# Performance work log

Measured on AMD Instinct MI355X. Metric: run time of the kernel, lower is better.

## Reference

```python
import jax, jax.numpy as jnp
import numpy as np

NS, NP, EJ, ER = 10000, 2048, 32768, 32768  # skills, job/resume pairs, edges
D, H = 1536, 8
NEG_SLOPE_ATT = 0.2   # GAT attention leaky_relu
NEG_SLOPE = 0.01      # F.leaky_relu / nn.LeakyReLU default


def setup_inputs() -> dict:
    key = jax.random.key(0)
    ks = jax.random.split(key, 20)
    rn = lambda k, shp, s=1.0: jax.random.normal(k, shp, dtype=jnp.float32) * s
    s_d = 1.0 / np.sqrt(D)
    return {
        "x_skill": rn(ks[0], (NS, D)),
        "x_job": rn(ks[1], (NP, D)),
        "x_resume": rn(ks[2], (NP, D)),
        # GraphConv params (lin_rel has bias, lin_root bias=False in PyG)
        "W_rel": rn(ks[3], (D, D), s_d),
        "b_rel": jnp.zeros((D,), jnp.float32),
        "W_root": rn(ks[4], (D, D), s_d),
        # GATConv params (heads=8, concat=False)
        "W_gat_src": rn(ks[5], (D, H * D), s_d),
        "W_gat_dst": rn(ks[6], (D, H * D), s_d),
        "att_src": rn(ks[7], (H, D), s_d),
        "att_dst": rn(ks[8], (H, D), s_d),
        "b_gat": jnp.zeros((D,), jnp.float32),
        # MLP: [3072 -> 512 -> 128 -> 1]
        "W1": rn(ks[9], (2 * D, 512), 1.0 / np.sqrt(2 * D)),
        "b1": jnp.zeros((512,), jnp.float32),
        "W2": rn(ks[10], (512, 128), 1.0 / np.sqrt(512)),
        "b2": jnp.zeros((128,), jnp.float32),
        "W3": rn(ks[11], (128, 1), 1.0 / np.sqrt(128)),
        "b3": jnp.zeros((1,), jnp.float32),
        # edge lists (src = skill idx, dst = job/resume idx)
        "edge_src_job": jax.random.randint(ks[12], (EJ,), 0, NS, dtype=jnp.int32),
        "edge_dst_job": jax.random.randint(ks[13], (EJ,), 0, NP, dtype=jnp.int32),
        "edge_src_res": jax.random.randint(ks[14], (ER,), 0, NS, dtype=jnp.int32),
        "edge_dst_res": jax.random.randint(ks[15], (ER,), 0, NP, dtype=jnp.int32),
    }


def reference(x_skill, x_job, x_resume, W_rel, b_rel, W_root,
              W_gat_src, W_gat_dst, att_src, att_dst, b_gat,
              W1, b1, W2, b2, W3, b3,
              edge_src_job, edge_dst_job, edge_src_res, edge_dst_res):
    n_pair = x_job.shape[0]

    # --- GraphConv (skill -> job): sum-aggregate then linear + root ---
    agg = jax.ops.segment_sum(x_skill[edge_src_job], edge_dst_job,
                              num_segments=n_pair)                  # [NP, D]
    h_job = agg @ W_rel + b_rel + x_job @ W_root                     # [NP, D]

    # --- GATConv (skill -> resume), heads=H, concat=False, no self-loops ---
    xs = (x_skill @ W_gat_src).reshape(-1, H, D)                     # [NS, H, D]
    xd = (x_resume @ W_gat_dst).reshape(-1, H, D)                    # [NP, H, D]
    a_src = jnp.einsum('nhd,hd->nh', xs, att_src)                    # [NS, H]
    a_dst = jnp.einsum('nhd,hd->nh', xd, att_dst)                    # [NP, H]
    e = jax.nn.leaky_relu(a_src[edge_src_res] + a_dst[edge_dst_res],
                          NEG_SLOPE_ATT)                             # [E, H]
    # segment softmax over edges grouped by destination resume node
    e_max = jax.ops.segment_max(e, edge_dst_res, num_segments=n_pair)
    e_exp = jnp.exp(e - e_max[edge_dst_res])
    denom = jax.ops.segment_sum(e_exp, edge_dst_res, num_segments=n_pair)
    alpha = e_exp / (denom[edge_dst_res] + 1e-16)                    # [E, H]
    msg = xs[edge_src_res] * alpha[:, :, None]                       # [E, H, D]
    out = jax.ops.segment_sum(msg, edge_dst_res, num_segments=n_pair)  # [NP, H, D]
    h_res = out.mean(axis=1) + b_gat                                 # concat=False -> head mean

    # --- combine + MLP ---
    h = jnp.concatenate([jax.nn.leaky_relu(h_job, NEG_SLOPE),
                         jax.nn.leaky_relu(h_res, NEG_SLOPE)], axis=1)  # [NP, 2D]
    h = jax.nn.leaky_relu(h @ W1 + b1, NEG_SLOPE)
    h = jax.nn.leaky_relu(h @ W2 + b2, NEG_SLOPE)
    score = (h @ W3 + b3).squeeze(-1)                                # [NP]
    return score, alpha
```

## Files before the change

### kernel.cpp

```cpp
#include <hip/hip_runtime.h>

#define D_ 1536
#define H_ 8

typedef __attribute__((ext_vector_type(8))) short bf16x8;
typedef __attribute__((ext_vector_type(4))) float f32x4;

__device__ __forceinline__ unsigned short f2bf(float f) {
    unsigned u = __builtin_bit_cast(unsigned, f);
    unsigned r = (u + 0x7fffu + ((u >> 16) & 1u)) >> 16;
    return (unsigned short)r;
}

__device__ __forceinline__ unsigned pack2bf(float a, float b) {
    return (unsigned)f2bf(a) | ((unsigned)f2bf(b) << 16);
}

__device__ __forceinline__ float bflo(unsigned u) { return __builtin_bit_cast(float, u << 16); }
__device__ __forceinline__ float bfhi(unsigned u) { return __builtin_bit_cast(float, u & 0xffff0000u); }

__device__ __forceinline__ void gload16(const void* g, void* l) {
    __builtin_amdgcn_global_load_lds((const __attribute__((address_space(1))) void*)g,
                                     (__attribute__((address_space(3))) void*)l, 16, 0, 0);
}

__global__ __launch_bounds__(256) void k_vmat2(const float* __restrict__ Wdst,
                                               const float* __restrict__ att_d,
                                               float* __restrict__ Vdst) {
    int d = blockIdx.x;
    const float4* wr = (const float4*)(Wdst + (size_t)d * (H_ * D_));
    int t = threadIdx.x;
    float part[H_];
    #pragma unroll
    for (int h = 0; h < H_; h++) {
        const float4* ar = (const float4*)(att_d + h * D_);
        float4 w0 = wr[h * 384 + t];
        float4 a0 = ar[t];
        float s = w0.x * a0.x + w0.y * a0.y + w0.z * a0.z + w0.w * a0.w;
        if (t < 128) {
            float4 w1 = wr[h * 384 + 256 + t];
            float4 a1 = ar[256 + t];
            s += w1.x * a1.x + w1.y * a1.y + w1.z * a1.z + w1.w * a1.w;
        }
        part[h] = s;
    }
    __shared__ float red[4][H_];
    int lane = t & 63, w = t >> 6;
    #pragma unroll
    for (int h = 0; h < H_; h++) {
        float v = part[h];
        for (int o = 32; o; o >>= 1) v += __shfl_down(v, o);
        if (lane == 0) red[w][h] = v;
    }
    __syncthreads();
    if (t < H_) Vdst[d * H_ + t] = red[0][t] + red[1][t] + red[2][t] + red[3][t];
}

__global__ __launch_bounds__(256) void k_a2(const float* __restrict__ xs,
                                            const float* __restrict__ xr,
                                            const float* __restrict__ Vs,
                                            const float* __restrict__ Vd,
                                            float* __restrict__ a_s,
                                            float* __restrict__ a_d,
                                            unsigned* __restrict__ xb, int NS) {
    int n = blockIdx.x;
    int skill = n < NS;
    int row = skill ? n : n - NS;
    const float2* xrow = (const float2*)(skill ? xs : xr) + (size_t)row * 768;
    const float* V = skill ? Vs : Vd;
    float* out = (skill ? a_s : a_d) + (size_t)row * H_;
    unsigned* ob = xb + (size_t)row * 768;
    float part[H_] = {};
    #pragma unroll
    for (int j = 0; j < 3; j++) {
        int e = threadIdx.x + j * 256;
        float2 v = xrow[e];
        if (skill) ob[e] = pack2bf(v.x, v.y);
        const float* vp = V + (size_t)(2 * e) * H_;
        #pragma unroll
        for (int h = 0; h < H_; h++) part[h] += v.x * vp[h] + v.y * vp[h + H_];
    }
    __shared__ float red[4][H_];
    int lane = threadIdx.x & 63, w = threadIdx.x >> 6;
    #pragma unroll
    for (int h = 0; h < H_; h++) {
        float v = part[h];
        for (int o = 32; o; o >>= 1) v += __shfl_down(v, o);
        if (lane == 0) red[w][h] = v;
    }
    __syncthreads();
    if (threadIdx.x < H_) out[threadIdx.x] =
        red[0][threadIdx.x] + red[1][threadIdx.x] + red[2][threadIdx.x] + red[3][threadIdx.x];
}

__global__ void k_count(const int* __restrict__ dj, int ej, const int* __restrict__ dr, int er,
                        int* cnt_j, int* cnt_r) {
    int i = blockIdx.x * blockDim.x + threadIdx.x;
    if (i < ej) atomicAdd(&cnt_j[dj[i]], 1);
    else if (i < ej + er) atomicAdd(&cnt_r[dr[i - ej]], 1);
}

__global__ void k_scan(const int* __restrict__ cnt_j, int* off_j,
                       const int* __restrict__ cnt_r, int* off_r, int NP) {
    const int* cnt = blockIdx.x ? cnt_r : cnt_j;
    int* off = blockIdx.x ? off_r : off_j;
    int lane = threadIdx.x;
    int chunk = (NP + 63) / 64;
    int base = lane * chunk;
    int sum = 0;
    for (int i = 0; i < chunk; i++) { int idx = base + i; if (idx < NP) sum += cnt[idx]; }
    int incl = sum;
    for (int o = 1; o < 64; o <<= 1) { int t = __shfl_up(incl, o); if (lane >= o) incl += t; }
    int run = incl - sum;
    for (int i = 0; i < chunk; i++) { int idx = base + i; if (idx < NP) { off[idx] = run; run += cnt[idx]; } }
    if (lane == 63) off[NP] = run;
}

__global__ void k_scatter(const int* __restrict__ dj, int ej, const int* __restrict__ dr, int er,
                          const int* __restrict__ off_j, int* fill_j, int* sid_j,
                          const int* __restrict__ off_r, int* fill_r, int* sid_r) {
    int i = blockIdx.x * blockDim.x + threadIdx.x;
    if (i < ej) {
        int p = dj[i];
        int slot = atomicAdd(&fill_j[p], 1);
        sid_j[off_j[p] + slot] = i;
    } else if (i < ej + er) {
        int e = i - ej;
        int p = dr[e];
        int slot = atomicAdd(&fill_r[p], 1);
        sid_r[off_r[p] + slot] = e;
    }
}

__global__ __launch_bounds__(256) void k_agg(const unsigned* __restrict__ xb, const int* __restrict__ src,
                                             const int* __restrict__ sid, const int* __restrict__ cnt,
                                             const int* __restrict__ off,
                                             const float* __restrict__ x_job,
                                             unsigned* __restrict__ cat_u) {
    int p = blockIdx.x, j = blockIdx.y;
    int n = cnt[p], o = off[p];
    int col = j * 256 + threadIdx.x;
    float2 acc = {0.f, 0.f};
    int i = 0;
    for (; i + 2 <= n; i += 2) {
        int e0 = sid[o + i], e1 = sid[o + i + 1];
        unsigned v0 = xb[(size_t)src[e0] * 768 + col];
        unsigned v1 = xb[(size_t)src[e1] * 768 + col];
        acc.x += bflo(v0) + bflo(v1);
        acc.y += bfhi(v0) + bfhi(v1);
    }
    if (i < n) {
        unsigned v = xb[(size_t)src[sid[o + i]] * 768 + col];
        acc.x += bflo(v); acc.y += bfhi(v);
    }
    unsigned* orow = cat_u + (size_t)p * 1536;
    orow[col] = pack2bf(acc.x, acc.y);
    float2 vj = ((const float2*)x_job)[(size_t)p * 768 + col];
    orow[768 + col] = pack2bf(vj.x, vj.y);
}

__global__ void k_softmax(const float* __restrict__ a_src, const float* __restrict__ a_dst,
                          const int* __restrict__ src, const int* __restrict__ sid,
                          const int* __restrict__ cnt, const int* __restrict__ off,
                          float* __restrict__ alpha_out) {
    int p = blockIdx.x;
    int n = cnt[p], o = off[p];
    if (n == 0) return;
    int lane = threadIdx.x;
    float4 ad0 = *(const float4*)(a_dst + (size_t)p * H_);
    float4 ad1 = *(const float4*)(a_dst + (size_t)p * H_ + 4);
    float adv[8] = {ad0.x, ad0.y, ad0.z, ad0.w, ad1.x, ad1.y, ad1.z, ad1.w};
    if (n <= 64) {
        int e = 0;
        float v[8];
        if (lane < n) {
            e = sid[o + lane];
            int s = src[e];
            float4 s0 = *(const float4*)(a_src + (size_t)s * H_);
            float4 s1 = *(const float4*)(a_src + (size_t)s * H_ + 4);
            float sv[8] = {s0.x, s0.y, s0.z, s0.w, s1.x, s1.y, s1.z, s1.w};
            #pragma unroll
            for (int h = 0; h < H_; h++) {
                float t = sv[h] + adv[h];
                v[h] = t >= 0.f ? t : 0.2f * t;
            }
        } else {
            #pragma unroll
            for (int h = 0; h < H_; h++) v[h] = -3.4e38f;
        }
        float ex[8];
        #pragma unroll
        for (int h = 0; h < H_; h++) {
            float m = v[h];
            for (int o2 = 32; o2; o2 >>= 1) m = fmaxf(m, __shfl_xor(m, o2));
            float ev = (lane < n) ? expf(v[h] - m) : 0.f;
            float s = ev;
            for (int o2 = 32; o2; o2 >>= 1) s += __shfl_xor(s, o2);
            ex[h] = ev / (s + 1e-16f);
        }
        if (lane < n) {
            *(float4*)(alpha_out + (size_t)e * H_) = make_float4(ex[0], ex[1], ex[2], ex[3]);
            *(float4*)(alpha_out + (size_t)e * H_ + 4) = make_float4(ex[4], ex[5], ex[6], ex[7]);
        }
    } else {
        #pragma unroll 1
        for (int h = 0; h < H_; h++) {
            float ad = adv[h];
            float m = -3.4e38f;
            for (int i = lane; i < n; i += 64) {
                int e = sid[o + i];
                float v = a_src[(size_t)src[e] * H_ + h] + ad;
                v = v >= 0.f ? v : 0.2f * v;
                m = fmaxf(m, v);
            }
            for (int o2 = 32; o2; o2 >>= 1) m = fmaxf(m, __shfl_xor(m, o2));
            float s = 0.f;
            for (int i = lane; i < n; i += 64) {
                int e = sid[o + i];
                float v = a_src[(size_t)src[e] * H_ + h] + ad;
                v = v >= 0.f ? v : 0.2f * v;
                s += expf(v - m);
            }
            for (int o2 = 32; o2; o2 >>= 1) s += __shfl_xor(s, o2);
            float inv = 1.f / (s + 1e-16f);
            for (int i = lane; i < n; i += 64) {
                int e = sid[o + i];
                float v = a_src[(size_t)src[e] * H_ + h] + ad;
                v = v >= 0.f ? v : 0.2f * v;
                alpha_out[(size_t)e * H_ + h] = expf(v - m) * inv;
            }
        }
    }
}

__global__ __launch_bounds__(256) void k_aggatt(const unsigned* __restrict__ xb,
                                                const float* __restrict__ alpha,
                                                const int* __restrict__ src, const int* __restrict__ sid,
                                                const int* __restrict__ cnt, const int* __restrict__ off,
                                                unsigned* __restrict__ aggatt_u) {
    int p = blockIdx.x, j = blockIdx.y;
    int n = cnt[p], o = off[p];
    int col = j * 256 + threadIdx.x;
    float2 acc[H_] = {};
    int i = 0;
    for (; i + 2 <= n; i += 2) {
        int e0 = sid[o + i], e1 = sid[o + i + 1];
        unsigned v0 = xb[(size_t)src[e0] * 768 + col];
        unsigned v1 = xb[(size_t)src[e1] * 768 + col];
        float l0 = bflo(v0), h0 = bfhi(v0), l1 = bflo(v1), h1 = bfhi(v1);
        const float* a0 = alpha + (size_t)e0 * H_;
        const float* a1 = alpha + (size_t)e1 * H_;
        #pragma unroll
        for (int h = 0; h < H_; h++) {
            float w0 = a0[h], w1 = a1[h];
            acc[h].x += w0 * l0 + w1 * l1;
            acc[h].y += w0 * h0 + w1 * h1;
        }
    }
    if (i < n) {
        int e0 = sid[o + i];
        unsigned v0 = xb[(size_t)src[e0] * 768 + col];
        float l0 = bflo(v0), h0 = bfhi(v0);
        const float* a0 = alpha + (size_t)e0 * H_;
        #pragma unroll
        for (int h = 0; h < H_; h++) { acc[h].x += a0[h] * l0; acc[h].y += a0[h] * h0; }
    }
    unsigned* orow = aggatt_u + (size_t)p * (H_ * 768);
    #pragma unroll
    for (int h = 0; h < H_; h++)
        orow[h * 768 + col] = pack2bf(acc[h].x, acc[h].y);
}

template <int GATB>
__global__ __launch_bounds__(256) void k_tr(const float* __restrict__ in, int ldin,
                                            unsigned short* __restrict__ out, int ldout,
                                            const float* __restrict__ att, float* __restrict__ V) {
    __shared__ float t[64][65];
    int k0 = blockIdx.y * 64, n0 = blockIdx.x * 64;
    int tx = threadIdx.x & 63, ty = threadIdx.x >> 6;
    #pragma unroll
    for (int i = 0; i < 16; i++) {
        int k = k0 + ty + i * 4;
        const float* rp;
        if (GATB) {
            int d2 = k % D_, h = k / D_;
            rp = in + (size_t)d2 * (H_ * D_) + (size_t)h * D_;
        } else {
            rp = in + (size_t)k * ldin;
        }
        t[ty + i * 4][tx] = rp[n0 + tx];
    }
    __syncthreads();
    int tx2 = threadIdx.x & 31, ty2 = threadIdx.x >> 5;
    #pragma unroll
    for (int i = 0; i < 8; i++) {
        int nl = ty2 + i * 8;
        unsigned v = pack2bf(t[tx2 * 2][nl], t[tx2 * 2 + 1][nl]);
        *(unsigned*)(out + (size_t)(n0 + nl) * ldout + k0 + tx2 * 2) = v;
    }
    if (GATB) {
        int h = k0 / D_, d2b = k0 - h * D_;
        int kl = threadIdx.x >> 2, q = threadIdx.x & 3;
        const float* ar = att + (size_t)h * D_ + n0 + q * 16;
        float s = 0.f;
        #pragma unroll
        for (int i = 0; i < 16; i++) s += t[kl][q * 16 + i] * ar[i];
        s += __shfl_xor(s, 1);
        s += __shfl_xor(s, 2);
        if (q == 0) atomicAdd(&V[(size_t)(d2b + kl) * H_ + h], s);
    }
}

__global__ __launch_bounds__(512, 4) void gemm_sk(const unsigned short* __restrict__ A, int lda,
                                                  const unsigned short* __restrict__ BT, int ldb,
                                                  float* __restrict__ P, int N, int bs, int extra) {
    __shared__ unsigned short As[3][256 * 32];
    __shared__ unsigned short Bs[3][128 * 32];
    int tid = threadIdx.x;
    int lane = tid & 63, wid = tid >> 6;

    int nwg = gridDim.x * gridDim.y;
    int bidh = blockIdx.y * gridDim.x + blockIdx.x;
    int swz = (bidh & 7) * (nwg >> 3) + (bidh >> 3);
    int bn = (swz % gridDim.x) * 128;
    int bm = (swz / gridDim.x) * 256;

    int z = blockIdx.z;
    int nt = bs + (z < extra);
    int kb = z * bs + min(z, extra);
    int kbase = kb * 32;

    int wr = wid >> 1, wc = wid & 1;
    int fr = lane & 15, g = lane >> 4;

    int ra0 = tid >> 2, sa0 = tid & 3;
    int ra1 = (tid + 512) >> 2;
    int sg_a0 = sa0 ^ ((ra0 >> 1) & 3);
    int sg_a1 = sa0 ^ ((ra1 >> 1) & 3);
    int sg_b = sg_a0;

    f32x4 acc[4][4] = {};

    auto stage = [&](int buf, int k0) {
        gload16(A + (size_t)(bm + ra0) * lda + k0 + sg_a0 * 8, &As[buf][tid * 8]);
        gload16(A + (size_t)(bm + ra1) * lda + k0 + sg_a1 * 8, &As[buf][(tid + 512) * 8]);
        gload16(BT + (size_t)(bn + ra0) * ldb + k0 + sg_b * 8, &Bs[buf][tid * 8]);
    };

    stage(0, kbase);
    if (nt > 1) stage(1, kbase + 32);
    for (int t = 0; t < nt; t++) {
        if (t + 2 < nt) {
            stage((t + 2) % 3, kbase + (t + 2) * 32);
            asm volatile("s_waitcnt vmcnt(6)" ::: "memory");
        } else if (t + 1 < nt) {
            asm volatile("s_waitcnt vmcnt(3)" ::: "memory");
        } else {
            asm volatile("s_waitcnt vmcnt(0)" ::: "memory");
        }
        __builtin_amdgcn_s_barrier();
        __builtin_amdgcn_sched_barrier(0);
        int cur = t % 3;
        bf16x8 a[4], b[4];
        #pragma unroll
        for (int mi = 0; mi < 4; mi++) {
            int row = wr * 64 + mi * 16 + fr;
            a[mi] = *(const bf16x8*)(&As[cur][row * 32 + ((g ^ ((row >> 1) & 3)) * 8)]);
        }
        #pragma unroll
        for (int ni = 0; ni < 4; ni++) {
            int row = wc * 64 + ni * 16 + fr;
            b[ni] = *(const bf16x8*)(&Bs[cur][row * 32 + ((g ^ ((row >> 1) & 3)) * 8)]);
        }
        __builtin_amdgcn_s_setprio(1);
        #pragma unroll
        for (int mi = 0; mi < 4; mi++)
            #pragma unroll
            for (int ni = 0; ni < 4; ni++)
                acc[mi][ni] = __builtin_amdgcn_mfma_f32_16x16x32_bf16(a[mi], b[ni], acc[mi][ni], 0, 0, 0);
        __builtin_amdgcn_s_setprio(0);
        __builtin_amdgcn_s_barrier();
        __builtin_amdgcn_sched_barrier(0);
    }

    size_t MN = (size_t)N * (size_t)(gridDim.y * 256);
    float* Pz = P + (size_t)z * MN;
    #pragma unroll
    for (int mi = 0; mi < 4; mi++) {
        int r0 = bm + wr * 64 + mi * 16 + (lane >> 4) * 4;
        #pragma unroll
        for (int ni = 0; ni < 4; ni++) {
            int c = bn + wc * 64 + ni * 16 + (lane & 15);
            #pragma unroll
            for (int j = 0; j < 4; j++)
                Pz[(size_t)(r0 + j) * N + c] = acc[mi][ni][j];
        }
    }
}

template <int OUT_BF16>
__global__ __launch_bounds__(256) void k_reduce(const float* __restrict__ P, int S, int MN, int N,
                                                void* __restrict__ Cout, int ldc,
                                                const float* __restrict__ bias, float scale,
                                                int useLeaky) {
    int idx = (blockIdx.x * 256 + threadIdx.x) * 4;
    if (idx >= MN) return;
    float4 v = *(const float4*)(P + idx);
    for (int s = 1; s < S; s++) {
        float4 t = *(const float4*)(P + (size_t)s * MN + idx);
        v.x += t.x; v.y += t.y; v.z += t.z; v.w += t.w;
    }
    int m = idx / N, n = idx - m * N;
    float vv[4] = {v.x, v.y, v.z, v.w};
    #pragma unroll
    for (int j = 0; j < 4; j++) {
        float x = vv[j] * scale + bias[n + j];
        if (useLeaky) x = x >= 0.f ? x : 0.01f * x;
        if (OUT_BF16) ((unsigned short*)Cout)[(size_t)m * ldc + n + j] = f2bf(x);
        else ((float*)Cout)[(size_t)m * ldc + n + j] = x;
    }
}

__global__ __launch_bounds__(256) void k_mlp2(const unsigned short* __restrict__ h1b,
                                              const float* __restrict__ W2,
                                              const float* __restrict__ b2,
                                              const float* __restrict__ W3,
                                              const float* __restrict__ b3,
                                              float* __restrict__ score) {
    __shared__ unsigned h1s[8][256];
    __shared__ float red[4][4];
    int p0 = blockIdx.x * 8;
    int tid = threadIdx.x;
    const unsigned* hsrc = (const unsigned*)h1b + (size_t)p0 * 256;
    #pragma unroll
    for (int i = 0; i < 8; i++) {
        int idx = tid + i * 256;
        h1s[idx >> 8][idx & 255] = hsrc[idx];
    }
    __syncthreads();
    int c = tid & 127, rg = tid >> 7;
    float acc[4] = {};
    for (int k = 0; k < 512; k += 2) {
        float w0 = W2[(size_t)k * 128 + c];
        float w1 = W2[(size_t)(k + 1) * 128 + c];
        #pragma unroll
        for (int r = 0; r < 4; r++) {
            unsigned hv = h1s[rg * 4 + r][k >> 1];
            acc[r] += bflo(hv) * w0 + bfhi(hv) * w1;
        }
    }
    float w3 = W3[c];
    float pr[4];
    #pragma unroll
    for (int r = 0; r < 4; r++) {
        float v = acc[r] + b2[c];
        v = v >= 0.f ? v : 0.01f * v;
        pr[r] = v * w3;
    }
    #pragma unroll
    for (int r = 0; r < 4; r++)
        for (int o = 32; o; o >>= 1) pr[r] += __shfl_down(pr[r], o);
    int w = tid >> 6;
    if ((tid & 63) == 0) {
        #pragma unroll
        for (int r = 0; r < 4; r++) red[w][r] = pr[r];
    }
    __syncthreads();
    if (tid < 8) {
        int rg2 = tid >> 2, r = tid & 3;
        float s = red[rg2 * 2][r] + red[rg2 * 2 + 1][r] + b3[0];
        score[p0 + rg2 * 4 + r] = s;
    }
}

extern "C" void kernel_launch(void* const* d_in, const int* in_sizes, int n_in,
                              void* d_out, int out_size, void* d_ws, size_t ws_size,
                              hipStream_t stream) {
    const float* x_skill = (const float*)d_in[0];
    const float* x_job   = (const float*)d_in[1];
    const float* x_resume= (const float*)d_in[2];
    const float* W_rel   = (const float*)d_in[3];
    const float* b_rel   = (const float*)d_in[4];
    const float* W_root  = (const float*)d_in[5];
    const float* W_gs    = (const float*)d_in[6];
    const float* W_gd    = (const float*)d_in[7];
    const float* att_s   = (const float*)d_in[8];
    const float* att_d   = (const float*)d_in[9];
    const float* b_gat   = (const float*)d_in[10];
    const float* W1      = (const float*)d_in[11];
    const float* b1      = (const float*)d_in[12];
    const float* W2      = (const float*)d_in[13];
    const float* b2      = (const float*)d_in[14];
    const float* W3      = (const float*)d_in[15];
    const float* b3      = (const float*)d_in[16];
    const int* esj = (const int*)d_in[17];
    const int* edj = (const int*)d_in[18];
    const int* esr = (const int*)d_in[19];
    const int* edr = (const int*)d_in[20];

    const int NS = in_sizes[0] / D_;
    const int NP = in_sizes[1] / D_;
    const int EJ = in_sizes[17];
    const int ER = in_sizes[19];

    float* score = (float*)d_out;
    float* alpha = score + NP;

    char* ws = (char*)d_ws;
    size_t off = 0;
    auto alloc = [&](size_t bytes) -> void* {
        void* p = ws + off;
        off = (off + bytes + 255) & ~(size_t)255;
        return p;
    };

    int* cnt_j  = (int*)alloc((size_t)4 * NP * sizeof(int));
    int* fill_j = cnt_j + NP;
    int* cnt_r  = cnt_j + 2 * NP;
    int* fill_r = cnt_j + 3 * NP;
    int* off_j  = (int*)alloc((size_t)(NP + 1) * sizeof(int));
    int* off_r  = (int*)alloc((size_t)(NP + 1) * sizeof(int));
    int* sid_j  = (int*)alloc((size_t)EJ * sizeof(int));
    int* sid_r  = (int*)alloc((size_t)ER * sizeof(int));
    float* Vsrc = (float*)alloc((size_t)D_ * H_ * 4);
    float* Vdst = (float*)alloc((size_t)D_ * H_ * 4);
    float* a_src= (float*)alloc((size_t)NS * H_ * 4);
    float* a_dst= (float*)alloc((size_t)NP * H_ * 4);
    unsigned short* cat_in = (unsigned short*)alloc((size_t)NP * 2 * D_ * 2);
    unsigned short* aggatt = (unsigned short*)alloc((size_t)NP * H_ * D_ * 2);
    unsigned short* BT1    = (unsigned short*)alloc((size_t)D_ * 2 * D_ * 2);
    unsigned short* BTg    = (unsigned short*)alloc((size_t)D_ * H_ * D_ * 2);
    unsigned short* BTw1   = (unsigned short*)alloc((size_t)512 * 2 * D_ * 2);
    unsigned short* hcat   = (unsigned short*)alloc((size_t)NP * 2 * D_ * 2);
    unsigned short* h1b    = (unsigned short*)alloc((size_t)NP * 512 * 2);
    float* Pbuf = (float*)alloc((size_t)5 * NP * D_ * 4);
    unsigned* xsb = (unsigned*)Pbuf;

    hipMemsetAsync(cnt_j, 0, (size_t)4 * NP * sizeof(int), stream);
    hipMemsetAsync(Vsrc, 0, (size_t)D_ * H_ * sizeof(float), stream);

    k_tr<0><<<dim3(D_ / 64, D_ / 64), 256, 0, stream>>>(W_rel, D_, BT1, 2 * D_, nullptr, nullptr);
    k_tr<0><<<dim3(D_ / 64, D_ / 64), 256, 0, stream>>>(W_root, D_, BT1 + D_, 2 * D_, nullptr, nullptr);
    k_tr<1><<<dim3(D_ / 64, (H_ * D_) / 64), 256, 0, stream>>>(W_gs, 0, BTg, H_ * D_, att_s, Vsrc);
    k_tr<0><<<dim3(512 / 64, (2 * D_) / 64), 256, 0, stream>>>(W1, 512, BTw1, 2 * D_, nullptr, nullptr);

    k_vmat2<<<D_, 256, 0, stream>>>(W_gd, att_d, Vdst);
    k_a2<<<NS + NP, 256, 0, stream>>>(x_skill, x_resume, Vsrc, Vdst, a_src, a_dst, xsb, NS);

    int egrid = (EJ + ER + 255) / 256;
    k_count<<<egrid, 256, 0, stream>>>(edj, EJ, edr, ER, cnt_j, cnt_r);
    k_scan<<<2, 64, 0, stream>>>(cnt_j, off_j, cnt_r, off_r, NP);
    k_scatter<<<egrid, 256, 0, stream>>>(edj, EJ, edr, ER, off_j, fill_j, sid_j, off_r, fill_r, sid_r);

    k_agg<<<dim3(NP, 3), 256, 0, stream>>>(xsb, esj, sid_j, cnt_j, off_j, x_job, (unsigned*)cat_in);
    k_softmax<<<NP, 64, 0, stream>>>(a_src, a_dst, esr, sid_r, cnt_r, off_r, alpha);
    k_aggatt<<<dim3(NP, 3), 256, 0, stream>>>(xsb, alpha, esr, sid_r, cnt_r, off_r, (unsigned*)aggatt);

    const int MN_f = NP * D_;
    const int MN_1 = NP * 512;

    gemm_sk<<<dim3(D_ / 128, NP / 256, 5), 512, 0, stream>>>(
        cat_in, 2 * D_, BT1, 2 * D_, Pbuf, D_, 19, 1);
    k_reduce<1><<<MN_f / 1024, 256, 0, stream>>>(Pbuf, 5, MN_f, D_, hcat, 2 * D_, b_rel, 1.f, 1);

    gemm_sk<<<dim3(D_ / 128, NP / 256, 5), 512, 0, stream>>>(
        aggatt, H_ * D_, BTg, H_ * D_, Pbuf, D_, 76, 4);
    k_reduce<1><<<MN_f / 1024, 256, 0, stream>>>(Pbuf, 5, MN_f, D_, hcat + D_, 2 * D_, b_gat, 1.f / H_, 1);

    gemm_sk<<<dim3(512 / 128, NP / 256, 8), 512, 0, stream>>>(
        hcat, 2 * D_, BTw1, 2 * D_, Pbuf, 512, 12, 0);
    k_reduce<1><<<MN_1 / 1024, 256, 0, stream>>>(Pbuf, 8, MN_1, 512, h1b, 512, b1, 1.f, 1);

    k_mlp2<<<NP / 8, 256, 0, stream>>>(h1b, W2, b2, W3, b3, score);
}
```

Measured before the change: 414.1 us.

## Store source ids in CSR order and fuse both aggregation kernels

The scatter kernel now writes each edge's source node index straight into the CSR-ordered arrays, so later kernels drop one level of indirection (edge id to src). Softmax also writes alpha in CSR order, which makes the per-node alpha reads in aggregation contiguous. The GraphConv and GAT aggregation kernels are merged into one launch with a 6-wide y grid, saving a launch and letting the two run at the same time. In exchange there is an extra alpha buffer and an extra write of alpha, and the merged blocks carry uneven amounts of work.

```diff
diff --git a/kernel.cpp b/kernel.cpp
--- a/kernel.cpp
+++ b/kernel.cpp
@@ -116,53 +116,29 @@
     if (lane == 63) off[NP] = run;
 }
 
-__global__ void k_scatter(const int* __restrict__ dj, int ej, const int* __restrict__ dr, int er,
-                          const int* __restrict__ off_j, int* fill_j, int* sid_j,
-                          const int* __restrict__ off_r, int* fill_r, int* sid_r) {
+__global__ void k_scatter(const int* __restrict__ dj, const int* __restrict__ sj, int ej,
+                          const int* __restrict__ dr, const int* __restrict__ sr, int er,
+                          const int* __restrict__ off_j, int* fill_j, int* srcv_j,
+                          const int* __restrict__ off_r, int* fill_r, int* sid_r, int* srcv_r) {
     int i = blockIdx.x * blockDim.x + threadIdx.x;
     if (i < ej) {
         int p = dj[i];
         int slot = atomicAdd(&fill_j[p], 1);
-        sid_j[off_j[p] + slot] = i;
+        srcv_j[off_j[p] + slot] = sj[i];
     } else if (i < ej + er) {
         int e = i - ej;
         int p = dr[e];
         int slot = atomicAdd(&fill_r[p], 1);
-        sid_r[off_r[p] + slot] = e;
-    }
-}
-
-__global__ __launch_bounds__(256) void k_agg(const unsigned* __restrict__ xb, const int* __restrict__ src,
-                                             const int* __restrict__ sid, const int* __restrict__ cnt,
-                                             const int* __restrict__ off,
-                                             const float* __restrict__ x_job,
-                                             unsigned* __restrict__ cat_u) {
-    int p = blockIdx.x, j = blockIdx.y;
-    int n = cnt[p], o = off[p];
-    int col = j * 256 + threadIdx.x;
-    float2 acc = {0.f, 0.f};
-    int i = 0;
-    for (; i + 2 <= n; i += 2) {
-        int e0 = sid[o + i], e1 = sid[o + i + 1];
-        unsigned v0 = xb[(size_t)src[e0] * 768 + col];
-        unsigned v1 = xb[(size_t)src[e1] * 768 + col];
-        acc.x += bflo(v0) + bflo(v1);
-        acc.y += bfhi(v0) + bfhi(v1);
-    }
-    if (i < n) {
-        unsigned v = xb[(size_t)src[sid[o + i]] * 768 + col];
-        acc.x += bflo(v); acc.y += bfhi(v);
-    }
-    unsigned* orow = cat_u + (size_t)p * 1536;
-    orow[col] = pack2bf(acc.x, acc.y);
-    float2 vj = ((const float2*)x_job)[(size_t)p * 768 + col];
-    orow[768 + col] = pack2bf(vj.x, vj.y);
+        int idx = off_r[p] + slot;
+        sid_r[idx] = e;
+        srcv_r[idx] = sr[e];
+    }
 }
 
 __global__ void k_softmax(const float* __restrict__ a_src, const float* __restrict__ a_dst,
-                          const int* __restrict__ src, const int* __restrict__ sid,
+                          const int* __restrict__ srcv, const int* __restrict__ sid,
                           const int* __restrict__ cnt, const int* __restrict__ off,
-                          float* __restrict__ alpha_out) {
+                          float* __restrict__ alpha_out, float* __restrict__ alpha_s) {
     int p = blockIdx.x;
     int n = cnt[p], o = off[p];
     if (n == 0) return;
@@ -175,7 +151,7 @@
         float v[8];
         if (lane < n) {
             e = sid[o + lane];
-            int s = src[e];
+            int s = srcv[o + lane];
             float4 s0 = *(const float4*)(a_src + (size_t)s * H_);
             float4 s1 = *(const float4*)(a_src + (size_t)s * H_ + 4);
             float sv[8] = {s0.x, s0.y, s0.z, s0.w, s1.x, s1.y, s1.z, s1.w};
@@ -201,6 +177,8 @@
         if (lane < n) {
             *(float4*)(alpha_out + (size_t)e * H_) = make_float4(ex[0], ex[1], ex[2], ex[3]);
             *(float4*)(alpha_out + (size_t)e * H_ + 4) = make_float4(ex[4], ex[5], ex[6], ex[7]);
+            *(float4*)(alpha_s + (size_t)(o + lane) * H_) = make_float4(ex[0], ex[1], ex[2], ex[3]);
+            *(float4*)(alpha_s + (size_t)(o + lane) * H_ + 4) = make_float4(ex[4], ex[5], ex[6], ex[7]);
         }
     } else {
         #pragma unroll 1
@@ -208,67 +186,90 @@
             float ad = adv[h];
             float m = -3.4e38f;
             for (int i = lane; i < n; i += 64) {
-                int e = sid[o + i];
-                float v = a_src[(size_t)src[e] * H_ + h] + ad;
+                float v = a_src[(size_t)srcv[o + i] * H_ + h] + ad;
                 v = v >= 0.f ? v : 0.2f * v;
                 m = fmaxf(m, v);
             }
             for (int o2 = 32; o2; o2 >>= 1) m = fmaxf(m, __shfl_xor(m, o2));
             float s = 0.f;
             for (int i = lane; i < n; i += 64) {
-                int e = sid[o + i];
-                float v = a_src[(size_t)src[e] * H_ + h] + ad;
+                float v = a_src[(size_t)srcv[o + i] * H_ + h] + ad;
                 v = v >= 0.f ? v : 0.2f * v;
                 s += expf(v - m);
             }
             for (int o2 = 32; o2; o2 >>= 1) s += __shfl_xor(s, o2);
             float inv = 1.f / (s + 1e-16f);
             for (int i = lane; i < n; i += 64) {
-                int e = sid[o + i];
-                float v = a_src[(size_t)src[e] * H_ + h] + ad;
+                float v = a_src[(size_t)srcv[o + i] * H_ + h] + ad;
                 v = v >= 0.f ? v : 0.2f * v;
-                alpha_out[(size_t)e * H_ + h] = expf(v - m) * inv;
+                float a = expf(v - m) * inv;
+                alpha_out[(size_t)sid[o + i] * H_ + h] = a;
+                alpha_s[(size_t)(o + i) * H_ + h] = a;
             }
         }
     }
 }
 
-__global__ __launch_bounds__(256) void k_aggatt(const unsigned* __restrict__ xb,
-                                                const float* __restrict__ alpha,
-                                                const int* __restrict__ src, const int* __restrict__ sid,
-                                                const int* __restrict__ cnt, const int* __restrict__ off,
-                                                unsigned* __restrict__ aggatt_u) {
-    int p = blockIdx.x, j = blockIdx.y;
-    int n = cnt[p], o = off[p];
-    int col = j * 256 + threadIdx.x;
-    float2 acc[H_] = {};
-    int i = 0;
-    for (; i + 2 <= n; i += 2) {
-        int e0 = sid[o + i], e1 = sid[o + i + 1];
-        unsigned v0 = xb[(size_t)src[e0] * 768 + col];
-        unsigned v1 = xb[(size_t)src[e1] * 768 + col];
-        float l0 = bflo(v0), h0 = bfhi(v0), l1 = bflo(v1), h1 = bfhi(v1);
-        const float* a0 = alpha + (size_t)e0 * H_;
-        const float* a1 = alpha + (size_t)e1 * H_;
-        #pragma unroll
-        for (int h = 0; h < H_; h++) {
-            float w0 = a0[h], w1 = a1[h];
-            acc[h].x += w0 * l0 + w1 * l1;
-            acc[h].y += w0 * h0 + w1 * h1;
-        }
-    }
-    if (i < n) {
-        int e0 = sid[o + i];
-        unsigned v0 = xb[(size_t)src[e0] * 768 + col];
-        float l0 = bflo(v0), h0 = bfhi(v0);
-        const float* a0 = alpha + (size_t)e0 * H_;
-        #pragma unroll
-        for (int h = 0; h < H_; h++) { acc[h].x += a0[h] * l0; acc[h].y += a0[h] * h0; }
-    }
-    unsigned* orow = aggatt_u + (size_t)p * (H_ * 768);
-    #pragma unroll
-    for (int h = 0; h < H_; h++)
-        orow[h * 768 + col] = pack2bf(acc[h].x, acc[h].y);
+__global__ __launch_bounds__(256) void k_aggs(const unsigned* __restrict__ xb,
+                                              const int* __restrict__ srcv_j,
+                                              const int* __restrict__ cnt_j, const int* __restrict__ off_j,
+                                              const int* __restrict__ srcv_r,
+                                              const int* __restrict__ cnt_r, const int* __restrict__ off_r,
+                                              const float* __restrict__ alpha_s,
+                                              const float* __restrict__ x_job,
+                                              unsigned* __restrict__ cat_u,
+                                              unsigned* __restrict__ aggatt_u) {
+    int p = blockIdx.x;
+    if (blockIdx.y < 3) {
+        int col = blockIdx.y * 256 + threadIdx.x;
+        int n = cnt_j[p], o = off_j[p];
+        float2 acc = {0.f, 0.f};
+        int i = 0;
+        for (; i + 2 <= n; i += 2) {
+            unsigned v0 = xb[(size_t)srcv_j[o + i] * 768 + col];
+            unsigned v1 = xb[(size_t)srcv_j[o + i + 1] * 768 + col];
+            acc.x += bflo(v0) + bflo(v1);
+            acc.y += bfhi(v0) + bfhi(v1);
+        }
+        if (i < n) {
+            unsigned v = xb[(size_t)srcv_j[o + i] * 768 + col];
+            acc.x += bflo(v); acc.y += bfhi(v);
+        }
+        unsigned* orow = cat_u + (size_t)p * 1536;
+        orow[col] = pack2bf(acc.x, acc.y);
+        float2 vj = ((const float2*)x_job)[(size_t)p * 768 + col];
+        orow[768 + col] = pack2bf(vj.x, vj.y);
+    } else {
+        int col = (blockIdx.y - 3) * 256 + threadIdx.x;
+        int n = cnt_r[p], o = off_r[p];
+        const float* as = alpha_s + (size_t)o * H_;
+        float2 acc[H_] = {};
+        int i = 0;
+        for (; i + 2 <= n; i += 2) {
+            unsigned v0 = xb[(size_t)srcv_r[o + i] * 768 + col];
+            unsigned v1 = xb[(size_t)srcv_r[o + i + 1] * 768 + col];
+            float l0 = bflo(v0), h0 = bfhi(v0), l1 = bflo(v1), h1 = bfhi(v1);
+            const float* a0 = as + (size_t)i * H_;
+            const float* a1 = a0 + H_;
+            #pragma unroll
+            for (int h = 0; h < H_; h++) {
+                float w0 = a0[h], w1 = a1[h];
+                acc[h].x += w0 * l0 + w1 * l1;
+                acc[h].y += w0 * h0 + w1 * h1;
+            }
+        }
+        if (i < n) {
+            unsigned v0 = xb[(size_t)srcv_r[o + i] * 768 + col];
+            float l0 = bflo(v0), h0 = bfhi(v0);
+            const float* a0 = as + (size_t)i * H_;
+            #pragma unroll
+            for (int h = 0; h < H_; h++) { acc[h].x += a0[h] * l0; acc[h].y += a0[h] * h0; }
+        }
+        unsigned* orow = aggatt_u + (size_t)p * (H_ * 768);
+        #pragma unroll
+        for (int h = 0; h < H_; h++)
+            orow[h * 768 + col] = pack2bf(acc[h].x, acc[h].y);
+    }
 }
 
 template <int GATB>
@@ -520,8 +521,10 @@
     int* fill_r = cnt_j + 3 * NP;
     int* off_j  = (int*)alloc((size_t)(NP + 1) * sizeof(int));
     int* off_r  = (int*)alloc((size_t)(NP + 1) * sizeof(int));
-    int* sid_j  = (int*)alloc((size_t)EJ * sizeof(int));
+    int* srcv_j = (int*)alloc((size_t)EJ * sizeof(int));
     int* sid_r  = (int*)alloc((size_t)ER * sizeof(int));
+    int* srcv_r = (int*)alloc((size_t)ER * sizeof(int));
+    float* alpha_s = (float*)alloc((size_t)ER * H_ * sizeof(float));
     float* Vsrc = (float*)alloc((size_t)D_ * H_ * 4);
     float* Vdst = (float*)alloc((size_t)D_ * H_ * 4);
     float* a_src= (float*)alloc((size_t)NS * H_ * 4);
@@ -550,11 +553,14 @@
     int egrid = (EJ + ER + 255) / 256;
     k_count<<<egrid, 256, 0, stream>>>(edj, EJ, edr, ER, cnt_j, cnt_r);
     k_scan<<<2, 64, 0, stream>>>(cnt_j, off_j, cnt_r, off_r, NP);
-    k_scatter<<<egrid, 256, 0, stream>>>(edj, EJ, edr, ER, off_j, fill_j, sid_j, off_r, fill_r, sid_r);
-
-    k_agg<<<dim3(NP, 3), 256, 0, stream>>>(xsb, esj, sid_j, cnt_j, off_j, x_job, (unsigned*)cat_in);
-    k_softmax<<<NP, 64, 0, stream>>>(a_src, a_dst, esr, sid_r, cnt_r, off_r, alpha);
-    k_aggatt<<<dim3(NP, 3), 256, 0, stream>>>(xsb, alpha, esr, sid_r, cnt_r, off_r, (unsigned*)aggatt);
+    k_scatter<<<egrid, 256, 0, stream>>>(edj, esj, EJ, edr, esr, ER,
+                                         off_j, fill_j, srcv_j,
+                                         off_r, fill_r, sid_r, srcv_r);
+
+    k_softmax<<<NP, 64, 0, stream>>>(a_src, a_dst, srcv_r, sid_r, cnt_r, off_r, alpha, alpha_s);
+    k_aggs<<<dim3(NP, 6), 256, 0, stream>>>(xsb, srcv_j, cnt_j, off_j,
+                                            srcv_r, cnt_r, off_r, alpha_s, x_job,
+                                            (unsigned*)cat_in, (unsigned*)aggatt);
 
     const int MN_f = NP * D_;
     const int MN_1 = NP * 512;
```

Measured after the change: 396.8 us. -4.2%, faster.
